# Optimization experiments

Hardware: AMD Instinct MI355X
Metric: run time of the kernel (lower is better)

Reference implementation:

```python
import jax, jax.numpy as jnp
import numpy as np

EPS = 1e-12
LORA_RANK = 16

def setup_inputs() -> dict:
    key = jax.random.key(0)
    ks = jax.random.split(key, 7)
    bs, sq, din, dout = 8, 2048, 2048, 2048
    n_tasks, n_splits, n_skills, r = 32, 1, 8, LORA_RANK
    return {
        'x': jax.random.normal(ks[0], (bs, sq, din), dtype=jnp.float32),
        'W': jax.random.normal(ks[1], (dout, din), dtype=jnp.float32) * (1.0 / np.sqrt(din)),
        'b': jax.random.normal(ks[2], (dout,), dtype=jnp.float32) * 0.02,
        'module_logits': jax.random.normal(ks[3], (n_tasks, n_splits * n_skills), dtype=jnp.float32) * 0.001,
        'A': jax.random.normal(ks[4], (n_splits, n_skills, din // n_splits, r), dtype=jnp.float32) * 0.02,
        'B': jax.random.normal(ks[5], (n_splits, n_skills, r, dout // n_splits), dtype=jnp.float32) * 0.02,
        'tasks': jax.random.randint(ks[6], (bs,), 0, n_tasks),
    }

def reference(x, W, b, module_logits, A, B, tasks):
    bs, sq, din = x.shape
    n_splits, n_skills, _, r = A.shape
    dout = W.shape[0]
    # Polytropon selector (eval mode): sigmoid + normalize over skills
    probs = jax.nn.sigmoid(module_logits[tasks]).reshape(bs, n_splits, n_skills)
    probs = probs / (probs.sum(-1, keepdims=True) + EPS)  # [bs, p, t]
    # WeightedSum combinor: per-example skill mixture of LoRA params
    A_c = jnp.einsum('bpt,ptir->bpir', probs, A)  # [bs, p, din/p, r]
    B_c = jnp.einsum('bpt,ptro->bpro', probs, B)  # [bs, p, r, dout/p]
    # LoRA forward: reshape to per-example [din, r] and [r, dout]
    A_r = A_c.reshape(bs, din, r)
    B_r = jnp.transpose(B_c, (0, 2, 1, 3)).reshape(bs, r, dout)
    lora = jnp.einsum('bsr,bro->bso', jnp.einsum('bsi,bir->bsr', x, A_r), B_r)
    base = jnp.einsum('bsi,oi->bso', x, W) + b
    return base + lora * (1.0 / r)
```

## Files before the change

kernel.cpp:

```cpp
#include <hip/hip_runtime.h>

typedef __attribute__((ext_vector_type(4))) float f32x4;
typedef __attribute__((ext_vector_type(8))) short bf16x8;

__device__ __forceinline__ unsigned short f2b(float f) {
  unsigned u = __float_as_uint(f);
  u = (u + 0x7FFFu + ((u >> 16) & 1u)) >> 16;
  return (unsigned short)u;
}

#define BAR() asm volatile("s_barrier" ::: "memory")
#define VMCNT(N) asm volatile("s_waitcnt vmcnt(" #N ")" ::: "memory")
#define SBAR0() __builtin_amdgcn_sched_barrier(0)

__global__ void combine_wconv_kernel(const float* __restrict__ logits,
                                     const int*   __restrict__ tasks,
                                     const float* __restrict__ A,
                                     const float* __restrict__ B,
                                     const float* __restrict__ W,
                                     unsigned short* __restrict__ Art,
                                     unsigned short* __restrict__ Brt,
                                     unsigned short* __restrict__ Wb)
{
  int blk = blockIdx.x;
  int tid = threadIdx.x;
  if (blk >= 64) {
    int idx0 = (blk - 64) * 256 + tid;
    #pragma unroll
    for (int c = 0; c < 32; ++c) {
      size_t i = ((size_t)idx0 + (size_t)c * 32768) * 4;
      f32x4 v = *(const f32x4*)(W + i);
      ushort4 o;
      o.x = f2b(v.x); o.y = f2b(v.y); o.z = f2b(v.z); o.w = f2b(v.w);
      *(ushort4*)(Wb + i) = o;
    }
    return;
  }
  int idx = blk * 256 + tid;
  int b = idx >> 11;
  int i = idx & 2047;
  int task = tasks[b];
  float p[8]; float s = 0.f;
  #pragma unroll
  for (int t = 0; t < 8; ++t) {
    float l = logits[task * 8 + t];
    float e = 1.f / (1.f + __expf(-l));
    p[t] = e; s += e;
  }
  float inv = 1.f / (s + 1e-12f);
  #pragma unroll
  for (int t = 0; t < 8; ++t) p[t] *= inv;

  float ar[16];
  #pragma unroll
  for (int r = 0; r < 16; ++r) ar[r] = 0.f;
  for (int t = 0; t < 8; ++t) {
    const float* ap = A + ((size_t)t * 2048 + i) * 16;
    float pt = p[t];
    #pragma unroll
    for (int r = 0; r < 16; ++r) ar[r] += pt * ap[r];
  }
  #pragma unroll
  for (int r = 0; r < 16; ++r)
    Art[((size_t)b * 16 + r) * 2048 + i] = f2b(ar[r]);

  float br[16];
  #pragma unroll
  for (int r = 0; r < 16; ++r) br[r] = 0.f;
  for (int t = 0; t < 8; ++t) {
    float pt = p[t];
    #pragma unroll
    for (int r = 0; r < 16; ++r) br[r] += pt * B[((size_t)t * 16 + r) * 2048 + i];
  }
  #pragma unroll
  for (int r = 0; r < 16; ++r)
    Brt[((size_t)b * 2048 + i) * 16 + r] = f2b(br[r] * 0.0625f);
}

__global__ void prep_kernel(const float* __restrict__ x,
                            const unsigned short* __restrict__ Art,
                            unsigned short* __restrict__ xb,
                            unsigned short* __restrict__ xa)
{
  __shared__ float red[4][16][16];
  int blk = blockIdx.x;
  int tid = threadIdx.x;
  int lane = tid & 63, wv = tid >> 6;
  int lr = lane & 15, hi = lane >> 4;
  int rowbase = blk * 16;
  int batch = rowbase >> 11;
  int row = rowbase + lr;
  f32x4 acc; acc.x = 0.f; acc.y = 0.f; acc.z = 0.f; acc.w = 0.f;
  const float* xrow = x + (size_t)row * 2048 + wv * 512 + hi * 8;
  unsigned short* xbrow = xb + (size_t)row * 2048 + wv * 512 + hi * 8;
  const unsigned short* artrow = Art + ((size_t)batch * 16 + lr) * 2048 + wv * 512 + hi * 8;
  #pragma unroll
  for (int ks = 0; ks < 16; ++ks) {
    f32x4 v0 = *(const f32x4*)(xrow + ks * 32);
    f32x4 v1 = *(const f32x4*)(xrow + ks * 32 + 4);
    bf16x8 av;
    av[0] = (short)f2b(v0.x); av[1] = (short)f2b(v0.y);
    av[2] = (short)f2b(v0.z); av[3] = (short)f2b(v0.w);
    av[4] = (short)f2b(v1.x); av[5] = (short)f2b(v1.y);
    av[6] = (short)f2b(v1.z); av[7] = (short)f2b(v1.w);
    *(bf16x8*)(xbrow + ks * 32) = av;
    bf16x8 bv = *(const bf16x8*)(artrow + ks * 32);
    acc = __builtin_amdgcn_mfma_f32_16x16x32_bf16(av, bv, acc, 0, 0, 0);
  }
  #pragma unroll
  for (int j = 0; j < 4; ++j) red[wv][hi * 4 + j][lr] = acc[j];
  __syncthreads();
  int rr = tid >> 4, cc = tid & 15;
  float s = red[0][rr][cc] + red[1][rr][cc] + red[2][rr][cc] + red[3][rr][cc];
  xa[(size_t)(rowbase + rr) * 16 + cc] = f2b(s);
}

__global__ __launch_bounds__(512)
void gemm_kernel(const unsigned short* __restrict__ xb,
                 const unsigned short* __restrict__ Wb,
                 const float* __restrict__ bias,
                 const unsigned short* __restrict__ xa,
                 const unsigned short* __restrict__ Brt,
                 float* __restrict__ out)
{
  __shared__ __align__(16) char lds[131072];
  const int tid = threadIdx.x;
  const int lane = tid & 63;
  const int wv = tid >> 6;
  const int wr = wv >> 2, wc = wv & 3;
  const int lr = lane & 15, hi = lane >> 4;
  const int hi16 = hi * 16;

  const int bid = blockIdx.x;
  const int swz = (bid & 7) * 64 + (bid >> 3);
  const int tm = swz >> 3, tn = swz & 7;
  const int rowbase = tm * 256, colbase = tn * 256;

  const int row0 = tid >> 3;
  const int cb0 = (tid & 7) * 16;
  const int scb_e = (cb0 ^ ((row0 & 7) << 4)) >> 1;
  const int rb5 = ((row0 >> 5) << 6) + (row0 & 31);

#define GL16(LDSOFF, GPTR) \
  __builtin_amdgcn_global_load_lds((const __attribute__((address_space(1))) unsigned int*)(GPTR), \
      (__attribute__((address_space(3))) unsigned int*)(lds + (LDSOFF)), 16, 0, 0)

#define STAGE_A(MH, DBUF, KOFF) { \
  const unsigned short* g_ = xb + (size_t)(rowbase + (MH)*64 + row0) * 2048 + (KOFF) + scb_e; \
  GL16((DBUF)*65536 + (MH)*16384 + tid*16, g_); \
  GL16((DBUF)*65536 + (MH)*16384 + 8192 + tid*16, g_ + 128*2048); \
}
#define STAGE_B(NH, DBUF, KOFF) { \
  const unsigned short* g_ = Wb + (size_t)(colbase + (NH)*32 + rb5) * 2048 + (KOFF) + scb_e; \
  GL16((DBUF)*65536 + 32768 + (NH)*16384 + tid*16, g_); \
  GL16((DBUF)*65536 + 32768 + (NH)*16384 + 8192 + tid*16, g_ + 128*2048); \
}

#define READ_A(MH, ABASE) \
  _Pragma("unroll") \
  for (int mf = 0; mf < 4; ++mf) { \
    int ar_ = (MH)*128 + wr*64 + mf*16 + lr; \
    _Pragma("unroll") \
    for (int kk = 0; kk < 2; ++kk) \
      a[mf][kk] = *(const bf16x8*)((ABASE) + ar_*128 + ((kk*64 + hi16) ^ ((ar_&7)<<4))); \
  }
#define READ_B(NH, BBASE, BREG) \
  _Pragma("unroll") \
  for (int nf = 0; nf < 2; ++nf) { \
    int br_ = (NH)*128 + wc*32 + nf*16 + lr; \
    _Pragma("unroll") \
    for (int kk = 0; kk < 2; ++kk) \
      BREG[nf][kk] = *(const bf16x8*)((BBASE) + br_*128 + ((kk*64 + hi16) ^ ((br_&7)<<4))); \
  }
#define MFMA_BLOCK(MH, NH, BREG) \
  __builtin_amdgcn_s_setprio(1); \
  _Pragma("unroll") \
  for (int mf = 0; mf < 4; ++mf) \
    _Pragma("unroll") \
    for (int nf = 0; nf < 2; ++nf) \
      _Pragma("unroll") \
      for (int kk = 0; kk < 2; ++kk) \
        acc[(MH)*4+mf][(NH)*2+nf] = __builtin_amdgcn_mfma_f32_16x16x32_bf16( \
            a[mf][kk], BREG[nf][kk], acc[(MH)*4+mf][(NH)*2+nf], 0, 0, 0); \
  __builtin_amdgcn_s_setprio(0);

  f32x4 acc[8][4];
  #pragma unroll
  for (int i = 0; i < 8; ++i)
    #pragma unroll
    for (int n = 0; n < 4; ++n) { acc[i][n].x = 0.f; acc[i][n].y = 0.f; acc[i][n].z = 0.f; acc[i][n].w = 0.f; }

  bf16x8 a[4][2], b0[2][2], b1[2][2];

  STAGE_A(0, 0, 0);
  STAGE_B(0, 0, 0);
  STAGE_A(1, 0, 0);
  STAGE_B(1, 0, 0);
  STAGE_A(0, 1, 64);
  STAGE_B(0, 1, 64);
  VMCNT(4);
  BAR();
  READ_A(0, lds);
  READ_B(0, lds + 32768, b0);

  for (int kt = 0; kt < 32; ++kt) {
    const int buf = kt & 1, nbuf = buf ^ 1;
    const char* Ab  = lds + buf * 65536;
    const char* Bb  = Ab + 32768;
    const char* Abn = lds + nbuf * 65536;
    const char* Bbn = Abn + 32768;
    const int k1 = (kt + 1) * 64, k2 = (kt + 2) * 64;

    BAR();
    READ_B(1, Bb, b1);
    if (kt < 31) STAGE_A(1, nbuf, k1);
    SBAR0();
    MFMA_BLOCK(0, 0, b0);

    BAR();
    if (kt < 31) STAGE_B(1, nbuf, k1);
    SBAR0();
    MFMA_BLOCK(0, 1, b1);
    READ_A(1, Ab);
    if (kt < 31) { VMCNT(4); }

    BAR();
    if (kt < 30) STAGE_A(0, buf, k2);
    SBAR0();
    MFMA_BLOCK(1, 0, b0);
    if (kt < 31) READ_B(0, Bbn, b0);

    BAR();
    if (kt < 30) STAGE_B(0, buf, k2);
    SBAR0();
    MFMA_BLOCK(1, 1, b1);
    if (kt < 31) READ_A(0, Abn);
    if (kt < 30) { VMCNT(4); }
    else if (kt == 30) { VMCNT(0); }
  }

  const int batch = rowbase >> 11;
  bf16x8 zf = (bf16x8)(short)0;
  bf16x8 ea[8], eb[4];
  #pragma unroll
  for (int i = 0; i < 8; ++i) {
    if (hi < 2)
      ea[i] = *(const bf16x8*)(xa + (size_t)(rowbase + wr * 128 + i * 16 + lr) * 16 + hi * 8);
    else
      ea[i] = zf;
  }
  #pragma unroll
  for (int n = 0; n < 4; ++n) {
    if (hi < 2)
      eb[n] = *(const bf16x8*)(Brt + ((size_t)batch * 2048 + colbase + wc * 64 + n * 16 + lr) * 16 + hi * 8);
    else
      eb[n] = zf;
  }
  #pragma unroll
  for (int i = 0; i < 8; ++i)
    #pragma unroll
    for (int n = 0; n < 4; ++n)
      acc[i][n] = __builtin_amdgcn_mfma_f32_16x16x32_bf16(ea[i], eb[n], acc[i][n], 0, 0, 0);

  #pragma unroll
  for (int n = 0; n < 4; ++n) {
    int col = colbase + wc * 64 + n * 16 + lr;
    float bbv = bias[col];
    #pragma unroll
    for (int i = 0; i < 8; ++i) {
      int r0 = rowbase + wr * 128 + i * 16 + hi * 4;
      #pragma unroll
      for (int j = 0; j < 4; ++j)
        out[(size_t)(r0 + j) * 2048 + col] = acc[i][n][j] + bbv;
    }
  }
#undef GL16
#undef STAGE_A
#undef STAGE_B
#undef READ_A
#undef READ_B
#undef MFMA_BLOCK
}

extern "C" void kernel_launch(void* const* d_in, const int* in_sizes, int n_in,
                              void* d_out, int out_size, void* d_ws, size_t ws_size,
                              hipStream_t stream) {
  const float* x      = (const float*)d_in[0];
  const float* W      = (const float*)d_in[1];
  const float* bias   = (const float*)d_in[2];
  const float* logits = (const float*)d_in[3];
  const float* A      = (const float*)d_in[4];
  const float* B      = (const float*)d_in[5];
  const int*   tasks  = (const int*)d_in[6];
  float* out = (float*)d_out;

  char* ws = (char*)d_ws;
  unsigned short* xb  = (unsigned short*)(ws);
  unsigned short* Wb  = (unsigned short*)(ws + 67108864);
  unsigned short* xa  = (unsigned short*)(ws + 67108864 + 8388608);
  unsigned short* Art = (unsigned short*)(ws + 67108864 + 8388608 + 524288);
  unsigned short* Brt = (unsigned short*)(ws + 67108864 + 8388608 + 1048576);

  combine_wconv_kernel<<<192, 256, 0, stream>>>(logits, tasks, A, B, W, Art, Brt, Wb);
  prep_kernel<<<1024, 256, 0, stream>>>(x, Art, xb, xa);
  gemm_kernel<<<512, 512, 0, stream>>>(xb, Wb, bias, xa, Brt, out);
}
```

Measured before the change: 185.9 us.

## Fuse fp32-to-bf16 conversion of x into GEMM A-tile staging

```diff
diff --git a/kernel.cpp b/kernel.cpp
--- a/kernel.cpp
+++ b/kernel.cpp
@@ -11,6 +11,7 @@
 
 #define BAR() asm volatile("s_barrier" ::: "memory")
 #define VMCNT(N) asm volatile("s_waitcnt vmcnt(" #N ")" ::: "memory")
+#define LGKM0() asm volatile("s_waitcnt lgkmcnt(0)" ::: "memory")
 #define SBAR0() __builtin_amdgcn_sched_barrier(0)
 
 __global__ void combine_wconv_kernel(const float* __restrict__ logits,
@@ -77,10 +78,9 @@
     Brt[((size_t)b * 2048 + i) * 16 + r] = f2b(br[r] * 0.0625f);
 }
 
-__global__ void prep_kernel(const float* __restrict__ x,
-                            const unsigned short* __restrict__ Art,
-                            unsigned short* __restrict__ xb,
-                            unsigned short* __restrict__ xa)
+__global__ void xa_kernel(const float* __restrict__ x,
+                          const unsigned short* __restrict__ Art,
+                          unsigned short* __restrict__ xa)
 {
   __shared__ float red[4][16][16];
   int blk = blockIdx.x;
@@ -92,7 +92,6 @@
   int row = rowbase + lr;
   f32x4 acc; acc.x = 0.f; acc.y = 0.f; acc.z = 0.f; acc.w = 0.f;
   const float* xrow = x + (size_t)row * 2048 + wv * 512 + hi * 8;
-  unsigned short* xbrow = xb + (size_t)row * 2048 + wv * 512 + hi * 8;
   const unsigned short* artrow = Art + ((size_t)batch * 16 + lr) * 2048 + wv * 512 + hi * 8;
   #pragma unroll
   for (int ks = 0; ks < 16; ++ks) {
@@ -103,7 +102,6 @@
     av[2] = (short)f2b(v0.z); av[3] = (short)f2b(v0.w);
     av[4] = (short)f2b(v1.x); av[5] = (short)f2b(v1.y);
     av[6] = (short)f2b(v1.z); av[7] = (short)f2b(v1.w);
-    *(bf16x8*)(xbrow + ks * 32) = av;
     bf16x8 bv = *(const bf16x8*)(artrow + ks * 32);
     acc = __builtin_amdgcn_mfma_f32_16x16x32_bf16(av, bv, acc, 0, 0, 0);
   }
@@ -115,8 +113,8 @@
   xa[(size_t)(rowbase + rr) * 16 + cc] = f2b(s);
 }
 
-__global__ __launch_bounds__(512)
-void gemm_kernel(const unsigned short* __restrict__ xb,
+__global__ __launch_bounds__(512, 2)
+void gemm_kernel(const float* __restrict__ x,
                  const unsigned short* __restrict__ Wb,
                  const float* __restrict__ bias,
                  const unsigned short* __restrict__ xa,
@@ -132,8 +130,9 @@
   const int hi16 = hi * 16;
 
   const int bid = blockIdx.x;
-  const int swz = (bid & 7) * 64 + (bid >> 3);
-  const int tm = swz >> 3, tn = swz & 7;
+  const int xcd = bid & 7, q = bid >> 3;
+  const int tm = xcd * 8 + (q >> 3);
+  const int tn = q & 7;
   const int rowbase = tm * 256, colbase = tn * 256;
 
   const int row0 = tid >> 3;
@@ -141,36 +140,62 @@
   const int scb_e = (cb0 ^ ((row0 & 7) << 4)) >> 1;
   const int rb5 = ((row0 >> 5) << 6) + (row0 & 31);
 
+  int aoffk[4];
+  #pragma unroll
+  for (int g = 0; g < 4; ++g) {
+    int off = wv * 4096 + g * 1024 + lane * 16;
+    int arow = off >> 7;
+    int scb = (off & 127) ^ ((arow & 7) << 4);
+    aoffk[g] = arow * 2048 + (scb >> 1);
+  }
+  const float* xbase = x + (size_t)rowbase * 2048;
+  const int aphys0 = wv * 4096 + lane * 16;
+
 #define GL16(LDSOFF, GPTR) \
   __builtin_amdgcn_global_load_lds((const __attribute__((address_space(1))) unsigned int*)(GPTR), \
       (__attribute__((address_space(3))) unsigned int*)(lds + (LDSOFF)), 16, 0, 0)
 
-#define STAGE_A(MH, DBUF, KOFF) { \
-  const unsigned short* g_ = xb + (size_t)(rowbase + (MH)*64 + row0) * 2048 + (KOFF) + scb_e; \
-  GL16((DBUF)*65536 + (MH)*16384 + tid*16, g_); \
-  GL16((DBUF)*65536 + (MH)*16384 + 8192 + tid*16, g_ + 128*2048); \
-}
 #define STAGE_B(NH, DBUF, KOFF) { \
   const unsigned short* g_ = Wb + (size_t)(colbase + (NH)*32 + rb5) * 2048 + (KOFF) + scb_e; \
   GL16((DBUF)*65536 + 32768 + (NH)*16384 + tid*16, g_); \
   GL16((DBUF)*65536 + 32768 + (NH)*16384 + 8192 + tid*16, g_ + 128*2048); \
 }
 
-#define READ_A(MH, ABASE) \
+#define LOAD_A2(G0, KO) { \
+  _Pragma("unroll") \
+  for (int g = (G0); g < (G0) + 2; ++g) { \
+    const float* p_ = xbase + aoffk[g] + (KO); \
+    va[2*g]   = *(const f32x4*)(p_); \
+    va[2*g+1] = *(const f32x4*)(p_ + 4); \
+  } \
+}
+#define WRITE_A2(G0, NBUF) { \
+  _Pragma("unroll") \
+  for (int g = (G0); g < (G0) + 2; ++g) { \
+    bf16x8 w_; \
+    w_[0]=(short)f2b(va[2*g].x);   w_[1]=(short)f2b(va[2*g].y); \
+    w_[2]=(short)f2b(va[2*g].z);   w_[3]=(short)f2b(va[2*g].w); \
+    w_[4]=(short)f2b(va[2*g+1].x); w_[5]=(short)f2b(va[2*g+1].y); \
+    w_[6]=(short)f2b(va[2*g+1].z); w_[7]=(short)f2b(va[2*g+1].w); \
+    *(bf16x8*)(lds + (NBUF)*65536 + aphys0 + g*1024) = w_; \
+  } \
+}
+
+#define READ_A(MH, BUF) \
   _Pragma("unroll") \
   for (int mf = 0; mf < 4; ++mf) { \
-    int ar_ = (MH)*128 + wr*64 + mf*16 + lr; \
+    int ar_ = wr*128 + (MH)*64 + mf*16 + lr; \
     _Pragma("unroll") \
     for (int kk = 0; kk < 2; ++kk) \
-      a[mf][kk] = *(const bf16x8*)((ABASE) + ar_*128 + ((kk*64 + hi16) ^ ((ar_&7)<<4))); \
-  }
-#define READ_B(NH, BBASE, BREG) \
+      a[mf][kk] = *(const bf16x8*)(lds + (BUF)*65536 + ar_*128 + ((kk*64 + hi16) ^ ((ar_&7)<<4))); \
+  }
+#define READ_B(NH, BUF, BREG) \
   _Pragma("unroll") \
   for (int nf = 0; nf < 2; ++nf) { \
     int br_ = (NH)*128 + wc*32 + nf*16 + lr; \
     _Pragma("unroll") \
     for (int kk = 0; kk < 2; ++kk) \
-      BREG[nf][kk] = *(const bf16x8*)((BBASE) + br_*128 + ((kk*64 + hi16) ^ ((br_&7)<<4))); \
+      BREG[nf][kk] = *(const bf16x8*)(lds + (BUF)*65536 + 32768 + br_*128 + ((kk*64 + hi16) ^ ((br_&7)<<4))); \
   }
 #define MFMA_BLOCK(MH, NH, BREG) \
   __builtin_amdgcn_s_setprio(1); \
@@ -191,52 +216,42 @@
     for (int n = 0; n < 4; ++n) { acc[i][n].x = 0.f; acc[i][n].y = 0.f; acc[i][n].z = 0.f; acc[i][n].w = 0.f; }
 
   bf16x8 a[4][2], b0[2][2], b1[2][2];
-
-  STAGE_A(0, 0, 0);
+  f32x4 va[8];
+
   STAGE_B(0, 0, 0);
-  STAGE_A(1, 0, 0);
   STAGE_B(1, 0, 0);
-  STAGE_A(0, 1, 64);
-  STAGE_B(0, 1, 64);
-  VMCNT(4);
+  LOAD_A2(0, 0);
+  LOAD_A2(2, 0);
+  WRITE_A2(0, 0);
+  WRITE_A2(2, 0);
+  LGKM0();
+  VMCNT(0);
   BAR();
-  READ_A(0, lds);
-  READ_B(0, lds + 32768, b0);
 
   for (int kt = 0; kt < 32; ++kt) {
     const int buf = kt & 1, nbuf = buf ^ 1;
-    const char* Ab  = lds + buf * 65536;
-    const char* Bb  = Ab + 32768;
-    const char* Abn = lds + nbuf * 65536;
-    const char* Bbn = Abn + 32768;
-    const int k1 = (kt + 1) * 64, k2 = (kt + 2) * 64;
-
-    BAR();
-    READ_B(1, Bb, b1);
-    if (kt < 31) STAGE_A(1, nbuf, k1);
+    const int k1 = (kt + 1) * 64;
+
+    if (kt < 31) {
+      STAGE_B(0, nbuf, k1);
+      STAGE_B(1, nbuf, k1);
+      LOAD_A2(0, k1);
+    }
+    READ_A(0, buf);
+    READ_B(0, buf, b0);
+    READ_B(1, buf, b1);
     SBAR0();
     MFMA_BLOCK(0, 0, b0);
-
+    if (kt < 31) LOAD_A2(2, k1);
+    MFMA_BLOCK(0, 1, b1);
+    READ_A(1, buf);
+    MFMA_BLOCK(1, 0, b0);
+    if (kt < 31) WRITE_A2(0, nbuf);
+    MFMA_BLOCK(1, 1, b1);
+    if (kt < 31) WRITE_A2(2, nbuf);
+    LGKM0();
+    if (kt < 31) { VMCNT(0); }
     BAR();
-    if (kt < 31) STAGE_B(1, nbuf, k1);
-    SBAR0();
-    MFMA_BLOCK(0, 1, b1);
-    READ_A(1, Ab);
-    if (kt < 31) { VMCNT(4); }
-
-    BAR();
-    if (kt < 30) STAGE_A(0, buf, k2);
-    SBAR0();
-    MFMA_BLOCK(1, 0, b0);
-    if (kt < 31) READ_B(0, Bbn, b0);
-
-    BAR();
-    if (kt < 30) STAGE_B(0, buf, k2);
-    SBAR0();
-    MFMA_BLOCK(1, 1, b1);
-    if (kt < 31) READ_A(0, Abn);
-    if (kt < 30) { VMCNT(4); }
-    else if (kt == 30) { VMCNT(0); }
   }
 
   const int batch = rowbase >> 11;
@@ -275,8 +290,9 @@
     }
   }
 #undef GL16
-#undef STAGE_A
 #undef STAGE_B
+#undef LOAD_A2
+#undef WRITE_A2
 #undef READ_A
 #undef READ_B
 #undef MFMA_BLOCK
@@ -295,13 +311,12 @@
   float* out = (float*)d_out;
 
   char* ws = (char*)d_ws;
-  unsigned short* xb  = (unsigned short*)(ws);
   unsigned short* Wb  = (unsigned short*)(ws + 67108864);
   unsigned short* xa  = (unsigned short*)(ws + 67108864 + 8388608);
   unsigned short* Art = (unsigned short*)(ws + 67108864 + 8388608 + 524288);
   unsigned short* Brt = (unsigned short*)(ws + 67108864 + 8388608 + 1048576);
 
   combine_wconv_kernel<<<192, 256, 0, stream>>>(logits, tasks, A, B, W, Art, Brt, Wb);
-  prep_kernel<<<1024, 256, 0, stream>>>(x, Art, xb, xa);
-  gemm_kernel<<<512, 512, 0, stream>>>(xb, Wb, bias, xa, Brt, out);
-}
+  xa_kernel<<<1024, 256, 0, stream>>>(x, Art, xa);
+  gemm_kernel<<<512, 512, 0, stream>>>(x, Wb, bias, xa, Brt, out);
+}
```

Result: no change. 188.1 us (+1.2%).
